# Kernel tuning notes

Hardware: AMD Instinct MI355X
Metric: run time of the kernel (lower is better)

Reference implementation:

```python
import jax, jax.numpy as jnp
import numpy as np

N_EMBD = 1024
N_HEAD = 16
HEAD_SIZE = N_EMBD // N_HEAD
EPS = 1e-5

def layer_norm(x, g, b):
    mu = jnp.mean(x, axis=-1, keepdims=True)
    var = jnp.mean(jnp.square(x - mu), axis=-1, keepdims=True)
    return (x - mu) * jax.lax.rsqrt(var + EPS) * g + b

def setup_inputs() -> dict:
    key = jax.random.key(0)
    ks = jax.random.split(key, 12)
    B, T, C, H, D = 2, 2048, N_EMBD, N_HEAD, HEAD_SIZE
    s = C ** -0.5
    return {
        "x":  jax.random.normal(ks[0], (B, T, C), jnp.float32),
        "Wq": jax.random.normal(ks[1], (H, C, D), jnp.float32) * s,
        "Wk": jax.random.normal(ks[2], (H, C, D), jnp.float32) * s,
        "Wv": jax.random.normal(ks[3], (H, C, D), jnp.float32) * s,
        "Wo": jax.random.normal(ks[4], (C, C), jnp.float32) * s,
        "bo": jnp.zeros((C,), jnp.float32),
        "g1": jnp.ones((C,), jnp.float32),
        "b1": jnp.zeros((C,), jnp.float32),
        "g2": jnp.ones((C,), jnp.float32),
        "b2": jnp.zeros((C,), jnp.float32),
        "W1": jax.random.normal(ks[5], (C, 4 * C), jnp.float32) * s,
        "bb1": jnp.zeros((4 * C,), jnp.float32),
        "W2": jax.random.normal(ks[6], (4 * C, C), jnp.float32) * (4 * C) ** -0.5,
        "bb2": jnp.zeros((C,), jnp.float32),
    }

def reference(x, Wq, Wk, Wv, Wo, bo, g1, b1, g2, b2, W1, bb1, W2, bb2):
    B, T, C = x.shape
    h = layer_norm(x, g1, b1)
    # per-head projections (no bias), stacked over heads: [B,H,T,D]
    q = jnp.einsum('btc,hcd->bhtd', h, Wq)
    k = jnp.einsum('btc,hcd->bhtd', h, Wk)
    v = jnp.einsum('btc,hcd->bhtd', h, Wv)
    # NOTE: original scales by C**-0.5 where C = n_embd (not head_size)
    scores = jnp.einsum('bhtd,bhsd->bhts', q, k) * (C ** -0.5)
    causal = jnp.tril(jnp.ones((T, T), dtype=bool))
    scores = jnp.where(causal, scores, -jnp.inf)
    wei = jax.nn.softmax(scores, axis=-1)
    y = jnp.einsum('bhts,bhsd->bhtd', wei, v)            # [B,H,T,D]
    y = jnp.transpose(y, (0, 2, 1, 3)).reshape(B, T, C)  # concat heads
    attn_out = y @ Wo + bo
    x = x + attn_out
    h2 = layer_norm(x, g2, b2)
    mlp = jax.nn.gelu(h2 @ W1 + bb1, approximate=True) @ W2 + bb2
    return x + mlp
```

## Files before the change

### kernel.cpp

```cpp
#include <hip/hip_runtime.h>
#include <cstdint>

typedef unsigned short u16;
typedef __attribute__((ext_vector_type(8))) short bf16x8;
typedef __attribute__((ext_vector_type(4))) float f32x4;

__device__ __forceinline__ u16 f2b(float f) {
  union { float f; unsigned u; } v; v.f = f;
  return (u16)((v.u + 0x7FFFu + ((v.u >> 16) & 1u)) >> 16);
}

__device__ __forceinline__ void async_copy16(void* lds, const void* g) {
  auto* l3 = reinterpret_cast<__attribute__((address_space(3))) unsigned int*>(
      reinterpret_cast<uintptr_t>(lds));
  auto* g1 = reinterpret_cast<const __attribute__((address_space(1))) unsigned int*>(
      reinterpret_cast<uintptr_t>(g));
  __builtin_amdgcn_global_load_lds(g1, l3, 16, 0, 0);
}

template<int MODE>
__global__ void gemm_bt(const u16* __restrict__ A, const u16* __restrict__ BT,
                        int M, int N, int K,
                        const float* __restrict__ bias,
                        const float* __restrict__ resid,
                        void* __restrict__ outp, float qs)
{
  __shared__ __align__(16) u16 sA[2][128 * 32];
  __shared__ __align__(16) u16 sB[2][128 * 32];
  const int tid = threadIdx.x;
  const int wid = tid >> 6;
  const int lane = tid & 63;
  const int L = lane & 15;
  const int Qd = lane >> 4;
  const int waveM = wid >> 1, waveN = wid & 1;
  const int bm = blockIdx.y * 128;
  const int bn = blockIdx.x * 128;

  f32x4 acc[4][4] = {};

  const int s0 = wid * 128 + lane;
  const int r0 = s0 >> 2, g0 = (s0 & 3) ^ ((r0 >> 1) & 3);
  const int s1 = s0 + 64;
  const int r1 = s1 >> 2, g1c = (s1 & 3) ^ ((r1 >> 1) & 3);
  const u16* Ar0 = A + (size_t)(bm + r0) * K + g0 * 8;
  const u16* Ar1 = A + (size_t)(bm + r1) * K + g1c * 8;
  const u16* Br0 = BT + (size_t)(bn + r0) * K + g0 * 8;
  const u16* Br1 = BT + (size_t)(bn + r1) * K + g1c * 8;

  const int nk = K >> 5;
  auto stage = [&](int it, int buf) {
    const int ko = it * 32;
    async_copy16(&sA[buf][(wid * 128) * 8],      Ar0 + ko);
    async_copy16(&sA[buf][(wid * 128 + 64) * 8], Ar1 + ko);
    async_copy16(&sB[buf][(wid * 128) * 8],      Br0 + ko);
    async_copy16(&sB[buf][(wid * 128 + 64) * 8], Br1 + ko);
  };

  stage(0, 0);
#pragma unroll 1
  for (int it = 0; it < nk; ++it) {
    const int buf = it & 1;
    __syncthreads();
    if (it + 1 < nk) stage(it + 1, buf ^ 1);

    bf16x8 af[4], bfr[4];
#pragma unroll
    for (int mt = 0; mt < 4; ++mt) {
      int r = waveM * 64 + mt * 16 + L;
      int slot = r * 4 + (Qd ^ ((r >> 1) & 3));
      af[mt] = *(const bf16x8*)&sA[buf][slot * 8];
    }
#pragma unroll
    for (int nt = 0; nt < 4; ++nt) {
      int r = waveN * 64 + nt * 16 + L;
      int slot = r * 4 + (Qd ^ ((r >> 1) & 3));
      bfr[nt] = *(const bf16x8*)&sB[buf][slot * 8];
    }
#pragma unroll
    for (int mt = 0; mt < 4; ++mt)
#pragma unroll
      for (int nt = 0; nt < 4; ++nt)
        acc[mt][nt] = __builtin_amdgcn_mfma_f32_16x16x32_bf16(af[mt], bfr[nt], acc[mt][nt], 0, 0, 0);
  }

#pragma unroll
  for (int mt = 0; mt < 4; ++mt) {
#pragma unroll
    for (int nt = 0; nt < 4; ++nt) {
#pragma unroll
      for (int i = 0; i < 4; ++i) {
        int m = bm + waveM * 64 + mt * 16 + Qd * 4 + i;
        int n = bn + waveN * 64 + nt * 16 + L;
        float c = acc[mt][nt][i];
        if constexpr (MODE == 0) {
          float sc = (n < 1024) ? qs : 1.0f;
          ((u16*)outp)[(size_t)m * N + n] = f2b(c * sc);
        } else if constexpr (MODE == 1) {
          ((u16*)outp)[(size_t)(n >> 11) * 2097152 + (size_t)m * 2048 + (n & 2047)] = f2b(c);
        } else if constexpr (MODE == 2) {
          size_t idx = (size_t)m * N + n;
          ((float*)outp)[idx] = resid[idx] + c + bias[n];
        } else {
          float v = c + bias[n];
          float t = v + 0.044715f * v * v * v;
          float gl = 0.5f * v * (1.0f + tanhf(0.7978845608028654f * t));
          ((u16*)outp)[(size_t)m * N + n] = f2b(gl);
        }
      }
    }
  }
}

__global__ void attn_kernel(const u16* __restrict__ qk, const u16* __restrict__ vT,
                            u16* __restrict__ y)
{
  __shared__ __align__(16) u16 sK[2][64 * 64];
  __shared__ __align__(16) u16 sV[2][64 * 64];
  __shared__ __align__(16) u16 sP[4 * 16 * 72];
  const int tid = threadIdx.x, wid = tid >> 6, lane = tid & 63;
  const int L = lane & 15, Qd = lane >> 4;
  const int bh = blockIdx.y, b = bh >> 4, h = bh & 15;

  const int s0 = wid * 128 + lane;
  const int rr0 = s0 >> 3, gg0 = (s0 & 7) ^ ((rr0 >> 1) & 7);
  const int s1 = s0 + 64;
  const int rr1 = s1 >> 3, gg1 = (s1 & 7) ^ ((rr1 >> 1) & 7);

  const u16* kb0 = qk + (size_t)(b * 2048 + rr0) * 2048 + 1024 + h * 64 + gg0 * 8;
  const u16* kb1 = qk + (size_t)(b * 2048 + rr1) * 2048 + 1024 + h * 64 + gg1 * 8;
  const u16* vb0 = vT + (size_t)(bh * 64 + rr0) * 2048 + gg0 * 8;
  const u16* vb1 = vT + (size_t)(bh * 64 + rr1) * 2048 + gg1 * 8;

  auto stage = [&](int kt, int buf) {
    const size_t ko = (size_t)kt * 64 * 2048;
    async_copy16(&sK[buf][(wid * 128) * 8],      kb0 + ko);
    async_copy16(&sK[buf][(wid * 128 + 64) * 8], kb1 + ko);
    async_copy16(&sV[buf][(wid * 128) * 8],      vb0 + kt * 64);
    async_copy16(&sV[buf][(wid * 128 + 64) * 8], vb1 + kt * 64);
  };

#pragma unroll 1
  for (int phase = 0; phase < 2; ++phase) {
    const int qt = phase == 0 ? (int)blockIdx.x : 31 - (int)blockIdx.x;
    const int nkt = qt + 1;

    const int qrow = b * 2048 + qt * 64 + wid * 16 + L;
    bf16x8 aq[2];
#pragma unroll
    for (int kk = 0; kk < 2; ++kk)
      aq[kk] = *(const bf16x8*)&qk[(size_t)qrow * 2048 + h * 64 + kk * 32 + Qd * 8];

    f32x4 oacc[4] = {};
    float lrow[4] = {0.f, 0.f, 0.f, 0.f};

    __syncthreads();
    stage(0, 0);

#pragma unroll 1
    for (int kt = 0; kt < nkt; ++kt) {
      const int buf = kt & 1;
      __syncthreads();
      if (kt + 1 < nkt) stage(kt + 1, buf ^ 1);

      f32x4 sacc[4] = {};
#pragma unroll
      for (int nt = 0; nt < 4; ++nt) {
        int r = nt * 16 + L;
#pragma unroll
        for (int kk = 0; kk < 2; ++kk) {
          int slot = r * 8 + ((kk * 4 + Qd) ^ ((r >> 1) & 7));
          bf16x8 bk = *(const bf16x8*)&sK[buf][slot * 8];
          sacc[nt] = __builtin_amdgcn_mfma_f32_16x16x32_bf16(aq[kk], bk, sacc[nt], 0, 0, 0);
        }
      }
      if (kt == qt) {
#pragma unroll
        for (int nt = 0; nt < 4; ++nt)
#pragma unroll
          for (int i = 0; i < 4; ++i)
            if (nt * 16 + L > wid * 16 + Qd * 4 + i) sacc[nt][i] = -__builtin_inff();
      }
#pragma unroll
      for (int nt = 0; nt < 4; ++nt)
#pragma unroll
        for (int i = 0; i < 4; ++i) {
          float p = exp2f(sacc[nt][i]);
          lrow[i] += p;
          sP[wid * 1152 + (Qd * 4 + i) * 72 + nt * 16 + L] = f2b(p);
        }
#pragma unroll
      for (int kk = 0; kk < 2; ++kk) {
        bf16x8 ap = *(const bf16x8*)&sP[wid * 1152 + L * 72 + kk * 32 + Qd * 8];
#pragma unroll
        for (int nt = 0; nt < 4; ++nt) {
          int r = nt * 16 + L;
          int slot = r * 8 + ((kk * 4 + Qd) ^ ((r >> 1) & 7));
          bf16x8 bv = *(const bf16x8*)&sV[buf][slot * 8];
          oacc[nt] = __builtin_amdgcn_mfma_f32_16x16x32_bf16(ap, bv, oacc[nt], 0, 0, 0);
        }
      }
    }

#pragma unroll
    for (int i = 0; i < 4; ++i) {
      float l = lrow[i];
      l += __shfl_xor(l, 1);
      l += __shfl_xor(l, 2);
      l += __shfl_xor(l, 4);
      l += __shfl_xor(l, 8);
      lrow[i] = l;
    }
#pragma unroll
    for (int nt = 0; nt < 4; ++nt)
#pragma unroll
      for (int i = 0; i < 4; ++i) {
        float o = oacc[nt][i] / lrow[i];
        int t = qt * 64 + wid * 16 + Qd * 4 + i;
        y[(size_t)(b * 2048 + t) * 1024 + h * 64 + nt * 16 + L] = f2b(o);
      }
  }
}

__global__ void ln_kernel(const float* __restrict__ x, const float* __restrict__ g,
                          const float* __restrict__ b, u16* __restrict__ out)
{
  const int row = blockIdx.x, tid = threadIdx.x;
  const float4 v = ((const float4*)(x + (size_t)row * 1024))[tid];
  float s = v.x + v.y + v.z + v.w;
  float s2 = v.x * v.x + v.y * v.y + v.z * v.z + v.w * v.w;
#pragma unroll
  for (int off = 1; off < 64; off <<= 1) {
    s += __shfl_xor(s, off);
    s2 += __shfl_xor(s2, off);
  }
  __shared__ float red[8];
  const int wid = tid >> 6, lane = tid & 63;
  if (lane == 0) { red[wid] = s; red[4 + wid] = s2; }
  __syncthreads();
  float S = red[0] + red[1] + red[2] + red[3];
  float S2 = red[4] + red[5] + red[6] + red[7];
  const float mu = S * (1.f / 1024.f);
  const float var = S2 * (1.f / 1024.f) - mu * mu;
  const float rs = rsqrtf(var + 1e-5f);
  const float4 gv = ((const float4*)g)[tid];
  const float4 bv = ((const float4*)b)[tid];
  ushort4 o;
  o.x = f2b((v.x - mu) * rs * gv.x + bv.x);
  o.y = f2b((v.y - mu) * rs * gv.y + bv.y);
  o.z = f2b((v.z - mu) * rs * gv.z + bv.z);
  o.w = f2b((v.w - mu) * rs * gv.w + bv.w);
  ((ushort4*)(out + (size_t)row * 1024))[tid] = o;
}

__global__ void transpose_cvt(const float* __restrict__ src, u16* __restrict__ dst,
                              int R, int C)
{
  __shared__ float tile[32][33];
  const int tx = threadIdx.x & 31, ty = threadIdx.x >> 5;
  const size_t zoff = (size_t)blockIdx.z * R * C;
  const int r0 = blockIdx.y * 32, c0 = blockIdx.x * 32;
#pragma unroll
  for (int k = 0; k < 4; ++k)
    tile[ty + k * 8][tx] = src[zoff + (size_t)(r0 + ty + k * 8) * C + c0 + tx];
  __syncthreads();
#pragma unroll
  for (int k = 0; k < 4; ++k)
    dst[zoff + (size_t)(c0 + ty + k * 8) * R + r0 + tx] = f2b(tile[tx][ty + k * 8]);
}

extern "C" void kernel_launch(void* const* d_in, const int* in_sizes, int n_in,
                              void* d_out, int out_size, void* d_ws, size_t ws_size,
                              hipStream_t stream)
{
  const float* x   = (const float*)d_in[0];
  const float* Wq  = (const float*)d_in[1];
  const float* Wk  = (const float*)d_in[2];
  const float* Wv  = (const float*)d_in[3];
  const float* Wo  = (const float*)d_in[4];
  const float* bo  = (const float*)d_in[5];
  const float* g1  = (const float*)d_in[6];
  const float* b1  = (const float*)d_in[7];
  const float* g2  = (const float*)d_in[8];
  const float* b2  = (const float*)d_in[9];
  const float* W1  = (const float*)d_in[10];
  const float* bb1 = (const float*)d_in[11];
  const float* W2  = (const float*)d_in[12];
  const float* bb2 = (const float*)d_in[13];

  char* ws = (char*)d_ws;
  const size_t MB = 1024 * 1024;
  u16*   h_bf  = (u16*)(ws);
  u16*   qkb   = (u16*)(ws + 8  * MB);
  u16*   vT    = (u16*)(ws + 24 * MB);
  u16*   y_bf  = (u16*)(ws + 32 * MB);
  float* x2    = (float*)(ws + 40 * MB);
  u16*   h2_bf = (u16*)(ws + 56 * MB);
  u16*   hid   = (u16*)(ws + 64 * MB);
  u16*   wqkv  = (u16*)(ws + 96 * MB);
  u16*   wo_bt = (u16*)(ws + 102 * MB);
  u16*   w1_bt = (u16*)(ws + 104 * MB);
  u16*   w2_bt = (u16*)(ws + 112 * MB);

  const float QSCALE = 0.04508422f;

  transpose_cvt<<<dim3(2, 32, 16), 256, 0, stream>>>(Wq, wqkv, 1024, 64);
  transpose_cvt<<<dim3(2, 32, 16), 256, 0, stream>>>(Wk, wqkv + 1024 * 1024, 1024, 64);
  transpose_cvt<<<dim3(2, 32, 16), 256, 0, stream>>>(Wv, wqkv + 2048 * 1024, 1024, 64);
  transpose_cvt<<<dim3(32, 32, 1), 256, 0, stream>>>(Wo, wo_bt, 1024, 1024);
  transpose_cvt<<<dim3(128, 32, 1), 256, 0, stream>>>(W1, w1_bt, 1024, 4096);
  transpose_cvt<<<dim3(32, 128, 1), 256, 0, stream>>>(W2, w2_bt, 4096, 1024);

  ln_kernel<<<4096, 256, 0, stream>>>(x, g1, b1, h_bf);
  gemm_bt<0><<<dim3(16, 32), 256, 0, stream>>>(h_bf, wqkv, 4096, 2048, 1024, nullptr, nullptr, qkb, QSCALE);
  gemm_bt<1><<<dim3(32, 8), 256, 0, stream>>>(wqkv + 2048 * 1024, h_bf, 1024, 4096, 1024, nullptr, nullptr, vT, 1.f);
  attn_kernel<<<dim3(16, 32), 256, 0, stream>>>(qkb, vT, y_bf);
  gemm_bt<2><<<dim3(8, 32), 256, 0, stream>>>(y_bf, wo_bt, 4096, 1024, 1024, bo, x, x2, 1.f);
  ln_kernel<<<4096, 256, 0, stream>>>(x2, g2, b2, h2_bf);
  gemm_bt<3><<<dim3(32, 32), 256, 0, stream>>>(h2_bf, w1_bt, 4096, 4096, 1024, bb1, nullptr, hid, 1.f);
  gemm_bt<2><<<dim3(8, 32), 256, 0, stream>>>(hid, w2_bt, 4096, 1024, 4096, bb2, x2, d_out, 1.f);
}
```

Baseline: 367.4 us.

## Fuse V projection into QKV GEMM and split-K the Wo/W2 GEMMs with atomics

Merges the separate V-transpose GEMM into the QK projection GEMM by widening N to 3072 and writing the V columns transposed with packed stores. The two N=1024 GEMMs (Wo and W2) are split along K into two halves over blockIdx.z and accumulate with float atomicAdd into an output that a new add-bias kernel pre-fills with residual plus bias. This doubles the block count for the narrow GEMMs to fill more CUs. The cost is atomic traffic, two extra elementwise kernel launches, and results whose summation order is nondeterministic.

```diff
diff --git a/kernel.cpp b/kernel.cpp
--- a/kernel.cpp
+++ b/kernel.cpp
@@ -18,12 +18,12 @@
   __builtin_amdgcn_global_load_lds(g1, l3, 16, 0, 0);
 }
 
-template<int MODE>
+template<int MODE, int KSPLIT>
 __global__ void gemm_bt(const u16* __restrict__ A, const u16* __restrict__ BT,
                         int M, int N, int K,
                         const float* __restrict__ bias,
-                        const float* __restrict__ resid,
-                        void* __restrict__ outp, float qs)
+                        void* __restrict__ outp, void* __restrict__ outp2,
+                        float qs)
 {
   __shared__ __align__(16) u16 sA[2][128 * 32];
   __shared__ __align__(16) u16 sB[2][128 * 32];
@@ -35,6 +35,7 @@
   const int waveM = wid >> 1, waveN = wid & 1;
   const int bm = blockIdx.y * 128;
   const int bn = blockIdx.x * 128;
+  const int koff = (KSPLIT == 2) ? (int)blockIdx.z * (K >> 1) : 0;
 
   f32x4 acc[4][4] = {};
 
@@ -42,12 +43,12 @@
   const int r0 = s0 >> 2, g0 = (s0 & 3) ^ ((r0 >> 1) & 3);
   const int s1 = s0 + 64;
   const int r1 = s1 >> 2, g1c = (s1 & 3) ^ ((r1 >> 1) & 3);
-  const u16* Ar0 = A + (size_t)(bm + r0) * K + g0 * 8;
-  const u16* Ar1 = A + (size_t)(bm + r1) * K + g1c * 8;
-  const u16* Br0 = BT + (size_t)(bn + r0) * K + g0 * 8;
-  const u16* Br1 = BT + (size_t)(bn + r1) * K + g1c * 8;
-
-  const int nk = K >> 5;
+  const u16* Ar0 = A + (size_t)(bm + r0) * K + koff + g0 * 8;
+  const u16* Ar1 = A + (size_t)(bm + r1) * K + koff + g1c * 8;
+  const u16* Br0 = BT + (size_t)(bn + r0) * K + koff + g0 * 8;
+  const u16* Br1 = BT + (size_t)(bn + r1) * K + koff + g1c * 8;
+
+  const int nk = (K / KSPLIT) >> 5;
   auto stage = [&](int it, int buf) {
     const int ko = it * 32;
     async_copy16(&sA[buf][(wid * 128) * 8],      Ar0 + ko);
@@ -87,24 +88,38 @@
   for (int mt = 0; mt < 4; ++mt) {
 #pragma unroll
     for (int nt = 0; nt < 4; ++nt) {
-#pragma unroll
-      for (int i = 0; i < 4; ++i) {
-        int m = bm + waveM * 64 + mt * 16 + Qd * 4 + i;
-        int n = bn + waveN * 64 + nt * 16 + L;
-        float c = acc[mt][nt][i];
-        if constexpr (MODE == 0) {
-          float sc = (n < 1024) ? qs : 1.0f;
-          ((u16*)outp)[(size_t)m * N + n] = f2b(c * sc);
-        } else if constexpr (MODE == 1) {
-          ((u16*)outp)[(size_t)(n >> 11) * 2097152 + (size_t)m * 2048 + (n & 2047)] = f2b(c);
-        } else if constexpr (MODE == 2) {
-          size_t idx = (size_t)m * N + n;
-          ((float*)outp)[idx] = resid[idx] + c + bias[n];
+      if constexpr (MODE == 0) {
+        if (bn < 2048) {
+#pragma unroll
+          for (int i = 0; i < 4; ++i) {
+            int m = bm + waveM * 64 + mt * 16 + Qd * 4 + i;
+            int n = bn + waveN * 64 + nt * 16 + L;
+            float sc = (n < 1024) ? qs : 1.0f;
+            ((u16*)outp)[(size_t)m * 2048 + n] = f2b(acc[mt][nt][i] * sc);
+          }
         } else {
-          float v = c + bias[n];
-          float t = v + 0.044715f * v * v * v;
-          float gl = 0.5f * v * (1.0f + tanhf(0.7978845608028654f * t));
-          ((u16*)outp)[(size_t)m * N + n] = f2b(gl);
+          int m0 = bm + waveM * 64 + mt * 16 + Qd * 4;
+          int n  = bn + waveN * 64 + nt * 16 + L;
+          u16 pk[4];
+#pragma unroll
+          for (int i = 0; i < 4; ++i) pk[i] = f2b(acc[mt][nt][i]);
+          size_t row = (size_t)((m0 >> 11) * 1024 + (n - 2048));
+          *(uint2*)&((u16*)outp2)[row * 2048 + (m0 & 2047)] = *(uint2*)pk;
+        }
+      } else {
+#pragma unroll
+        for (int i = 0; i < 4; ++i) {
+          int m = bm + waveM * 64 + mt * 16 + Qd * 4 + i;
+          int n = bn + waveN * 64 + nt * 16 + L;
+          float c = acc[mt][nt][i];
+          if constexpr (MODE == 3) {
+            float v = c + bias[n];
+            float t = v + 0.044715f * v * v * v;
+            float gl = 0.5f * v * (1.0f + tanhf(0.7978845608028654f * t));
+            ((u16*)outp)[(size_t)m * N + n] = f2b(gl);
+          } else {
+            atomicAdd(&((float*)outp)[(size_t)m * N + n], c);
+          }
         }
       }
     }
@@ -252,6 +267,18 @@
   ((ushort4*)(out + (size_t)row * 1024))[tid] = o;
 }
 
+__global__ void addbias_kernel(const float* __restrict__ src,
+                               const float* __restrict__ bias,
+                               float* __restrict__ dst)
+{
+  const int tid = blockIdx.x * 256 + threadIdx.x;
+  const float4 s = ((const float4*)src)[tid];
+  const float4 bv = ((const float4*)bias)[tid & 255];
+  float4 o;
+  o.x = s.x + bv.x; o.y = s.y + bv.y; o.z = s.z + bv.z; o.w = s.w + bv.w;
+  ((float4*)dst)[tid] = o;
+}
+
 __global__ void transpose_cvt(const float* __restrict__ src, u16* __restrict__ dst,
                               int R, int C)
 {
@@ -311,11 +338,12 @@
   transpose_cvt<<<dim3(32, 128, 1), 256, 0, stream>>>(W2, w2_bt, 4096, 1024);
 
   ln_kernel<<<4096, 256, 0, stream>>>(x, g1, b1, h_bf);
-  gemm_bt<0><<<dim3(16, 32), 256, 0, stream>>>(h_bf, wqkv, 4096, 2048, 1024, nullptr, nullptr, qkb, QSCALE);
-  gemm_bt<1><<<dim3(32, 8), 256, 0, stream>>>(wqkv + 2048 * 1024, h_bf, 1024, 4096, 1024, nullptr, nullptr, vT, 1.f);
+  gemm_bt<0, 1><<<dim3(24, 32), 256, 0, stream>>>(h_bf, wqkv, 4096, 3072, 1024, nullptr, qkb, vT, QSCALE);
   attn_kernel<<<dim3(16, 32), 256, 0, stream>>>(qkb, vT, y_bf);
-  gemm_bt<2><<<dim3(8, 32), 256, 0, stream>>>(y_bf, wo_bt, 4096, 1024, 1024, bo, x, x2, 1.f);
+  addbias_kernel<<<4096, 256, 0, stream>>>(x, bo, x2);
+  gemm_bt<4, 2><<<dim3(8, 32, 2), 256, 0, stream>>>(y_bf, wo_bt, 4096, 1024, 1024, nullptr, x2, nullptr, 1.f);
   ln_kernel<<<4096, 256, 0, stream>>>(x2, g2, b2, h2_bf);
-  gemm_bt<3><<<dim3(32, 32), 256, 0, stream>>>(h2_bf, w1_bt, 4096, 4096, 1024, bb1, nullptr, hid, 1.f);
-  gemm_bt<2><<<dim3(8, 32), 256, 0, stream>>>(hid, w2_bt, 4096, 1024, 4096, bb2, x2, d_out, 1.f);
-}
+  gemm_bt<3, 1><<<dim3(32, 32), 256, 0, stream>>>(h2_bf, w1_bt, 4096, 4096, 1024, bb1, hid, nullptr, 1.f);
+  addbias_kernel<<<4096, 256, 0, stream>>>(x2, bb2, (float*)d_out);
+  gemm_bt<4, 2><<<dim3(8, 32, 2), 256, 0, stream>>>(hid, w2_bt, 4096, 1024, 4096, nullptr, d_out, nullptr, 1.f);
+}
```

After: 395.5 us. 1.08x slower.
